# Optimization experiments

Measured on AMD Instinct MI355X. Metric: run time of the kernel, lower is better.

## Reference

```python
import jax, jax.numpy as jnp
import numpy as np

MAX_VAL = 1000000000000.0


def setup_inputs() -> dict:
    key = jax.random.key(0)
    k1, k2, k3, k4 = jax.random.split(key, 4)
    B, H, N, D = 2, 16, 2048, 64
    query = jax.random.normal(k1, (B, H, N, D), dtype=jnp.float32)
    key_t = jax.random.normal(k2, (B, H, N, D), dtype=jnp.float32)
    value = jax.random.normal(k3, (B, H, N, D), dtype=jnp.float32)
    mask = jax.random.randint(k4, (B, 1, 1, N), 0, 2).astype(bool)
    return {"query": query, "key": key_t, "value": value, "mask": mask,
            "global_num": 8, "window_size": 64}


def reference(query, key, value, mask, global_num, window_size):
    # query/key/value: [B, H, N, D]; mask: [B, 1, 1, N] bool (True = keep)
    B, H, N, D = query.shape
    scale = 1.0 / jnp.sqrt(jnp.asarray(D, dtype=query.dtype))

    # split heads: first global_num are global, rest are local (windowed)
    q_g, k_g, v_g = query[:, :global_num], key[:, :global_num], value[:, :global_num]
    q_l, k_l, v_l = query[:, global_num:], key[:, global_num:], value[:, global_num:]

    # ---- global heads: dense masked attention ----
    scores_g = jnp.einsum('bhqd,bhkd->bhqk', q_g, k_g) * scale
    scores_g = jnp.where(mask, scores_g, -MAX_VAL)
    p_g = jax.nn.softmax(scores_g, axis=-1)
    out_g = jnp.einsum('bhqk,bhkd->bhqd', p_g, v_l[:, :0]) if False else jnp.einsum('bhqk,bhkd->bhqd', p_g, v_g)

    # ---- local heads: window-banded mask on top of padding mask ----
    pos = jnp.arange(N)
    distance = jnp.abs(pos[None, :] - pos[:, None])  # [N, N]
    band = (distance <= window_size)                 # [N, N] bool
    mask_l = mask & band                             # [B, 1, N, N]
    scores_l = jnp.einsum('bhqd,bhkd->bhqk', q_l, k_l) * scale
    scores_l = jnp.where(mask_l, scores_l, -MAX_VAL)
    p_l = jax.nn.softmax(scores_l, axis=-1)
    out_l = jnp.einsum('bhqk,bhkd->bhqd', p_l, v_l)

    out = jnp.concatenate([out_g, out_l], axis=1)  # [B, H, N, D]
    return (out, p_g, p_l)
```

## Files before the change

### kernel.cpp

```cpp
#include <hip/hip_runtime.h>
#include <stdint.h>

typedef __attribute__((ext_vector_type(8))) __bf16 bf16x8;
typedef __attribute__((ext_vector_type(4))) float f32x4;
typedef __attribute__((ext_vector_type(4))) int i32x4;

#define DEVI static __device__ __forceinline__

constexpr int NN = 2048;
constexpr int DD = 64;
constexpr int NH = 16;
constexpr int NG = 8;
constexpr float SCALE = 0.125f;
constexpr float NEGBIG = -1.0e12f;
constexpr size_t OUT_ELEMS = (size_t)2 * NH * NN * DD;
constexpr size_t PG_ELEMS  = (size_t)2 * NG * NN * NN;
constexpr size_t T_ELEMS   = (size_t)2 * NH * NN * DD;
constexpr size_t WS_NEED   = 5 * T_ELEMS * sizeof(__bf16);

struct Frag { bf16x8 hi, lo; };

DEVI Frag make_frag(const float* p) {
  f32x4 a = *(const f32x4*)p;
  f32x4 b = *(const f32x4*)(p + 4);
  Frag f;
#pragma unroll
  for (int j = 0; j < 8; j++) {
    float x = (j < 4) ? a[j] : b[j - 4];
    __bf16 h = (__bf16)x;
    f.hi[j] = h;
    f.lo[j] = (__bf16)(x - (float)h);
  }
  return f;
}

DEVI f32x4 mfma(bf16x8 a, bf16x8 b, f32x4 c) {
  return __builtin_amdgcn_mfma_f32_16x16x32_bf16(a, b, c, 0, 0, 0);
}

DEVI void nt_store4(float* p, f32x4 v) {
  __builtin_nontemporal_store(v, (f32x4*)p);
}

struct KT { bf16x8 hi[2][2]; bf16x8 lo[2][2]; i32x4 mv[2]; };
struct VT { bf16x8 v[4]; };

template <bool PRE>
DEVI void load_kt(KT& kt, const __bf16* khi, const __bf16* klo,
                  const float* kp, const int* mp, int wc, int li, int qi) {
#pragma unroll
  for (int Mt = 0; Mt < 2; Mt++)
#pragma unroll
    for (int ks = 0; ks < 2; ks++) {
      const size_t off = (size_t)(wc + Mt * 16 + li) * DD + ks * 32 + qi * 8;
      if constexpr (PRE) {
        kt.hi[Mt][ks] = *(const bf16x8*)(khi + off);
        kt.lo[Mt][ks] = *(const bf16x8*)(klo + off);
      } else {
        Frag f = make_frag(kp + off);
        kt.hi[Mt][ks] = f.hi;
        kt.lo[Mt][ks] = f.lo;
      }
    }
  kt.mv[0] = *(const i32x4*)(mp + wc + qi * 4);
  kt.mv[1] = *(const i32x4*)(mp + wc + 16 + qi * 4);
}

template <bool PRE>
DEVI void load_vt(VT& vt, const __bf16* vtp, const float* vp, int wc, int li, int qi) {
  if constexpr (PRE) {
#pragma unroll
    for (int dt = 0; dt < 4; dt++)
      vt.v[dt] = *(const bf16x8*)(vtp + (size_t)(dt * 16 + li) * NN + wc + qi * 8);
  } else {
#pragma unroll
    for (int dt = 0; dt < 4; dt++)
#pragma unroll
      for (int j = 0; j < 8; j++)
        vt.v[dt][j] = (__bf16)vp[(size_t)(wc + qi * 8 + j) * DD + dt * 16 + li];
  }
}

template <bool LOC>
DEVI void tileA(const KT& kt, const Frag qf[2][2], int wc, int rb, int li, int qi,
                float* m, float* l) {
#pragma unroll
  for (int rs = 0; rs < 2; rs++) {
    f32x4 acc[2];
#pragma unroll
    for (int Mt = 0; Mt < 2; Mt++) {
      f32x4 c = {0.f, 0.f, 0.f, 0.f};
#pragma unroll
      for (int ks = 0; ks < 2; ks++) {
        c = mfma(kt.hi[Mt][ks], qf[rs][ks].hi, c);
        c = mfma(kt.hi[Mt][ks], qf[rs][ks].lo, c);
        c = mfma(kt.lo[Mt][ks], qf[rs][ks].hi, c);
      }
      acc[Mt] = c;
    }
    const int row = rb + rs * 16 + li;
    float vals[8];
#pragma unroll
    for (int Mt = 0; Mt < 2; Mt++)
#pragma unroll
      for (int r = 0; r < 4; r++) {
        const int col = wc + Mt * 16 + qi * 4 + r;
        bool ok = (kt.mv[Mt][r] != 0);
        if constexpr (LOC) { int d = row - col; if (d < 0) d = -d; ok = ok && (d <= 64); }
        vals[Mt * 4 + r] = ok ? acc[Mt][r] * SCALE : NEGBIG;
      }
    float mx = vals[0];
#pragma unroll
    for (int j = 1; j < 8; j++) mx = fmaxf(mx, vals[j]);
    const float mn = fmaxf(m[rs], mx);
    float s = 0.f;
#pragma unroll
    for (int j = 0; j < 8; j++) s += __expf(vals[j] - mn);
    l[rs] = l[rs] * __expf(m[rs] - mn) + s;
    m[rs] = mn;
  }
}

template <bool LOC>
DEVI void tileB(const KT& kt, const VT& vt, const Frag qf[2][2], int wc, int rb,
                int li, int qi, const float* m, const float* rl,
                f32x4 (&o)[2][4], float* pp, int srcA, int srcB, bool selB) {
#pragma unroll
  for (int rs = 0; rs < 2; rs++) {
    f32x4 acc[2];
#pragma unroll
    for (int Mt = 0; Mt < 2; Mt++) {
      f32x4 c = {0.f, 0.f, 0.f, 0.f};
#pragma unroll
      for (int ks = 0; ks < 2; ks++) {
        c = mfma(kt.hi[Mt][ks], qf[rs][ks].hi, c);
        c = mfma(kt.hi[Mt][ks], qf[rs][ks].lo, c);
        c = mfma(kt.lo[Mt][ks], qf[rs][ks].hi, c);
      }
      acc[Mt] = c;
    }
    const int row = rb + rs * 16 + li;
    float pf[8];
#pragma unroll
    for (int Mt = 0; Mt < 2; Mt++)
#pragma unroll
      for (int r = 0; r < 4; r++) {
        const int col = wc + Mt * 16 + qi * 4 + r;
        bool ok = (kt.mv[Mt][r] != 0);
        if constexpr (LOC) { int d = row - col; if (d < 0) d = -d; ok = ok && (d <= 64); }
        const float vv = ok ? acc[Mt][r] * SCALE : NEGBIG;
        pf[Mt * 4 + r] = __expf(vv - m[rs]) * rl[rs];
      }
    float pa[8];
#pragma unroll
    for (int j = 0; j < 8; j++) {
      const int src = (j < 4) ? srcA : srcB;
      const float v0 = __shfl(pf[0 + (j & 3)], src);
      const float v1 = __shfl(pf[4 + (j & 3)], src);
      pa[j] = selB ? v1 : v0;
    }
    float* prow = pp + (size_t)(rb + rs * 16 + li) * NN + wc + qi * 8;
    nt_store4(prow,     (f32x4){pa[0], pa[1], pa[2], pa[3]});
    nt_store4(prow + 4, (f32x4){pa[4], pa[5], pa[6], pa[7]});
    bf16x8 pb;
#pragma unroll
    for (int j = 0; j < 8; j++) pb[j] = (__bf16)pa[j];
#pragma unroll
    for (int dt = 0; dt < 4; dt++)
      o[rs][dt] = mfma(pb, vt.v[dt], o[rs][dt]);
  }
}

__global__ __launch_bounds__(256)
void prep(const float* __restrict__ Q, const float* __restrict__ K,
          const float* __restrict__ V, __bf16* __restrict__ W) {
  const int bid = blockIdx.x;
  if (bid < 4096) {
    const float* src = (bid < 2048) ? Q : K;
    __bf16* hi = W + ((bid < 2048) ? (size_t)0 : 2 * T_ELEMS);
    __bf16* lo = hi + T_ELEMS;
    const size_t base = ((size_t)(bid & 2047) * 256 + threadIdx.x) * 8;
    f32x4 a = *(const f32x4*)(src + base);
    f32x4 b = *(const f32x4*)(src + base + 4);
    bf16x8 h, l;
#pragma unroll
    for (int j = 0; j < 8; j++) {
      float x = (j < 4) ? a[j] : b[j - 4];
      __bf16 hh = (__bf16)x;
      h[j] = hh;
      l[j] = (__bf16)(x - (float)hh);
    }
    *(bf16x8*)(hi + base) = h;
    *(bf16x8*)(lo + base) = l;
  } else {
    __bf16* vt = W + 4 * T_ELEMS;
    const int t  = (bid - 4096) * 256 + (int)threadIdx.x;
    const int ng = t & 63;
    const int dh = t >> 6;
    const int d  = dh & 63;
    const int bh = dh >> 6;
    const float* vp = V + (size_t)bh * NN * DD;
    __bf16* dst = vt + ((size_t)bh * DD + d) * NN + ng * 32;
    bf16x8 o[4];
#pragma unroll
    for (int j = 0; j < 32; j++)
      o[j >> 3][j & 7] = (__bf16)vp[(size_t)(ng * 32 + j) * DD + d];
#pragma unroll
    for (int k = 0; k < 4; k++) *(bf16x8*)(dst + k * 8) = o[k];
  }
}

template <bool PRE>
__global__ __launch_bounds__(256, 4)
void wattn(const float* __restrict__ Q, const float* __restrict__ K,
           const float* __restrict__ V, const int* __restrict__ MSK,
           float* __restrict__ OUT, const __bf16* __restrict__ W) {
  __shared__ float2 mlS[4][32];
  __shared__ float  oS[4][16][64];

  const int bid0 = (int)blockIdx.x;
  const int xcd = bid0 & 7, jj = bid0 >> 3;
  const int bid = (jj < 128) ? (xcd * 128 + jj) : (1024 + xcd * 128 + (jj - 128));
  const bool loc = bid >= 1024;
  const int lb = loc ? bid - 1024 : bid;
  const int bh = lb >> 6;
  const int b  = bh >> 3;
  const int hh = bh & 7;
  const int h  = loc ? (hh + 8) : hh;
  const int rb = (lb & 63) * 32;
  const int wave = (int)(threadIdx.x >> 6);
  const int lane = (int)(threadIdx.x & 63);
  const int qi = lane >> 4;
  const int li = lane & 15;

  const size_t tb = ((size_t)(b * NH + h) * NN) * DD;
  const float* qp = Q + tb;
  const float* kp = K + tb;
  const float* vp = V + tb;
  const __bf16* qhi = W + tb;
  const __bf16* qlo = W + T_ELEMS + tb;
  const __bf16* khi = W + 2 * T_ELEMS + tb;
  const __bf16* klo = W + 3 * T_ELEMS + tb;
  const __bf16* vtp = W + 4 * T_ELEMS + (size_t)(b * NH + h) * DD * NN;
  const int*   mp = MSK + (size_t)b * NN;
  float* op = OUT + tb;
  float* pp = OUT + OUT_ELEMS + (loc ? PG_ELEMS : (size_t)0)
                  + ((size_t)(b * NG + hh) * NN) * NN;

  const int cb  = rb - 64;
  const int wlo = cb < 0 ? 0 : cb;
  const int whi = (rb + 96 > NN) ? NN : rb + 96;

  if (loc) {
    const int c0 = (int)threadIdx.x * 8;
    const f32x4 z = {0.f, 0.f, 0.f, 0.f};
#pragma unroll 1
    for (int rr = 0; rr < 32; rr++) {
      if (c0 >= wlo && c0 < whi) continue;
      float* dst = pp + (size_t)(rb + rr) * NN + c0;
      nt_store4(dst, z);
      nt_store4(dst + 4, z);
    }
  }

  Frag qf[2][2];
#pragma unroll
  for (int rs = 0; rs < 2; rs++)
#pragma unroll
    for (int ks = 0; ks < 2; ks++) {
      const size_t off = (size_t)(rb + rs * 16 + li) * DD + ks * 32 + qi * 8;
      if constexpr (PRE) {
        qf[rs][ks].hi = *(const bf16x8*)(qhi + off);
        qf[rs][ks].lo = *(const bf16x8*)(qlo + off);
      } else {
        qf[rs][ks] = make_frag(qp + off);
      }
    }

  float m[2] = {NEGBIG, NEGBIG};
  float l[2] = {0.f, 0.f};

  if (!loc) {
#pragma unroll 1
    for (int tt = 0; tt < 16; tt++) {
      const int wc = wave * 512 + tt * 32;
      KT kt;
      load_kt<PRE>(kt, khi, klo, kp, mp, wc, li, qi);
      tileA<false>(kt, qf, wc, rb, li, qi, m, l);
    }
  } else {
#pragma unroll 1
    for (int t = wave; t < 5; t += 4) {
      const int wc = cb + 32 * t;
      if ((unsigned)wc >= (unsigned)NN) continue;
      KT kt;
      load_kt<PRE>(kt, khi, klo, kp, mp, wc, li, qi);
      tileA<true>(kt, qf, wc, rb, li, qi, m, l);
    }
  }

#pragma unroll
  for (int rs = 0; rs < 2; rs++) {
#pragma unroll
    for (int off = 16; off <= 32; off <<= 1) {
      const float mo  = __shfl_xor(m[rs], off);
      const float lo2 = __shfl_xor(l[rs], off);
      const float mn  = fmaxf(m[rs], mo);
      l[rs] = l[rs] * __expf(m[rs] - mn) + lo2 * __expf(mo - mn);
      m[rs] = mn;
    }
    if (qi == 0) mlS[wave][rs * 16 + li] = make_float2(m[rs], l[rs]);
  }
  __syncthreads();

  float rl[2];
#pragma unroll
  for (int rs = 0; rs < 2; rs++) {
    float mm = NEGBIG, ll = 0.f;
#pragma unroll
    for (int w = 0; w < 4; w++) {
      const float2 p = mlS[w][rs * 16 + li];
      const float mn = fmaxf(mm, p.x);
      ll = ll * __expf(mm - mn) + p.y * __expf(p.x - mn);
      mm = mn;
    }
    m[rs] = mm;
    rl[rs] = 1.0f / ll;
  }

  f32x4 o[2][4];
#pragma unroll
  for (int rs = 0; rs < 2; rs++)
#pragma unroll
    for (int dt = 0; dt < 4; dt++) o[rs][dt] = (f32x4){0.f, 0.f, 0.f, 0.f};

  const int srcA = (((qi * 2) + 0) & 3) * 16 + li;
  const int srcB = (((qi * 2) + 1) & 3) * 16 + li;
  const bool selB = (qi >> 1) != 0;

  if (!loc) {
#pragma unroll 1
    for (int tt = 0; tt < 16; tt++) {
      const int wc = wave * 512 + tt * 32;
      KT kt;
      VT vt;
      load_kt<PRE>(kt, khi, klo, kp, mp, wc, li, qi);
      load_vt<PRE>(vt, vtp, vp, wc, li, qi);
      tileB<false>(kt, vt, qf, wc, rb, li, qi, m, rl, o, pp, srcA, srcB, selB);
    }
  } else {
#pragma unroll 1
    for (int t = wave; t < 5; t += 4) {
      const int wc = cb + 32 * t;
      if ((unsigned)wc >= (unsigned)NN) continue;
      KT kt;
      VT vt;
      load_kt<PRE>(kt, khi, klo, kp, mp, wc, li, qi);
      load_vt<PRE>(vt, vtp, vp, wc, li, qi);
      tileB<true>(kt, vt, qf, wc, rb, li, qi, m, rl, o, pp, srcA, srcB, selB);
    }
  }

  const int tid = (int)threadIdx.x;
  const int rr = tid >> 4;
  const int d0 = (tid & 15) * 4;
#pragma unroll
  for (int rs = 0; rs < 2; rs++) {
#pragma unroll
    for (int dt = 0; dt < 4; dt++)
#pragma unroll
      for (int r = 0; r < 4; r++)
        oS[wave][qi * 4 + r][dt * 16 + li] = o[rs][dt][r];
    __syncthreads();
    f32x4 s = {0.f, 0.f, 0.f, 0.f};
#pragma unroll
    for (int w = 0; w < 4; w++)
      s += *(const f32x4*)&oS[w][rr][d0];
    nt_store4(op + (size_t)(rb + rs * 16 + rr) * DD + d0, s);
    if (rs == 0) __syncthreads();
  }
}

extern "C" void kernel_launch(void* const* d_in, const int* in_sizes, int n_in,
                              void* d_out, int out_size, void* d_ws, size_t ws_size,
                              hipStream_t stream) {
  (void)in_sizes; (void)n_in; (void)out_size;
  const float* Q = (const float*)d_in[0];
  const float* K = (const float*)d_in[1];
  const float* V = (const float*)d_in[2];
  const int*   M = (const int*)d_in[3];
  float* O = (float*)d_out;
  if (ws_size >= WS_NEED && d_ws != nullptr) {
    __bf16* W = (__bf16*)d_ws;
    prep<<<dim3(4608), dim3(256), 0, stream>>>(Q, K, V, W);
    wattn<true><<<dim3(2048), dim3(256), 0, stream>>>(Q, K, V, M, O, W);
  } else {
    wattn<false><<<dim3(2048), dim3(256), 0, stream>>>(Q, K, V, M, O, nullptr);
  }
}
```

Before: 861.4 us.

## Split pass-B into per-row-subtile loops and use regular stores for outputs

The second pass now loops over the two 16-row subtiles one at a time, reloading only that subtile's Q fragments and keeping four output accumulators instead of eight. This lowers register pressure so occupancy can rise, but K/V tiles and the mask are loaded twice. Nontemporal stores for the probability matrices and the output are also replaced with ordinary stores.

New measurement: 888.9 us. 1.03x slower.

```diff
diff --git a/kernel.cpp b/kernel.cpp
--- a/kernel.cpp
+++ b/kernel.cpp
@@ -38,10 +38,6 @@
   return __builtin_amdgcn_mfma_f32_16x16x32_bf16(a, b, c, 0, 0, 0);
 }
 
-DEVI void nt_store4(float* p, f32x4 v) {
-  __builtin_nontemporal_store(v, (f32x4*)p);
-}
-
 struct KT { bf16x8 hi[2][2]; bf16x8 lo[2][2]; i32x4 mv[2]; };
 struct VT { bf16x8 v[4]; };
 
@@ -82,7 +78,7 @@
 }
 
 template <bool LOC>
-DEVI void tileA(const KT& kt, const Frag qf[2][2], int wc, int rb, int li, int qi,
+DEVI void tileA(const KT& kt, const Frag qa[2][2], int wc, int rb, int li, int qi,
                 float* m, float* l) {
 #pragma unroll
   for (int rs = 0; rs < 2; rs++) {
@@ -92,9 +88,9 @@
       f32x4 c = {0.f, 0.f, 0.f, 0.f};
 #pragma unroll
       for (int ks = 0; ks < 2; ks++) {
-        c = mfma(kt.hi[Mt][ks], qf[rs][ks].hi, c);
-        c = mfma(kt.hi[Mt][ks], qf[rs][ks].lo, c);
-        c = mfma(kt.lo[Mt][ks], qf[rs][ks].hi, c);
+        c = mfma(kt.hi[Mt][ks], qa[rs][ks].hi, c);
+        c = mfma(kt.hi[Mt][ks], qa[rs][ks].lo, c);
+        c = mfma(kt.lo[Mt][ks], qa[rs][ks].hi, c);
       }
       acc[Mt] = c;
     }
@@ -122,53 +118,50 @@
 }
 
 template <bool LOC>
-DEVI void tileB(const KT& kt, const VT& vt, const Frag qf[2][2], int wc, int rb,
-                int li, int qi, const float* m, const float* rl,
-                f32x4 (&o)[2][4], float* pp, int srcA, int srcB, bool selB) {
-#pragma unroll
-  for (int rs = 0; rs < 2; rs++) {
-    f32x4 acc[2];
-#pragma unroll
-    for (int Mt = 0; Mt < 2; Mt++) {
-      f32x4 c = {0.f, 0.f, 0.f, 0.f};
-#pragma unroll
-      for (int ks = 0; ks < 2; ks++) {
-        c = mfma(kt.hi[Mt][ks], qf[rs][ks].hi, c);
-        c = mfma(kt.hi[Mt][ks], qf[rs][ks].lo, c);
-        c = mfma(kt.lo[Mt][ks], qf[rs][ks].hi, c);
-      }
-      acc[Mt] = c;
-    }
-    const int row = rb + rs * 16 + li;
-    float pf[8];
-#pragma unroll
-    for (int Mt = 0; Mt < 2; Mt++)
-#pragma unroll
-      for (int r = 0; r < 4; r++) {
-        const int col = wc + Mt * 16 + qi * 4 + r;
-        bool ok = (kt.mv[Mt][r] != 0);
-        if constexpr (LOC) { int d = row - col; if (d < 0) d = -d; ok = ok && (d <= 64); }
-        const float vv = ok ? acc[Mt][r] * SCALE : NEGBIG;
-        pf[Mt * 4 + r] = __expf(vv - m[rs]) * rl[rs];
-      }
-    float pa[8];
-#pragma unroll
-    for (int j = 0; j < 8; j++) {
-      const int src = (j < 4) ? srcA : srcB;
-      const float v0 = __shfl(pf[0 + (j & 3)], src);
-      const float v1 = __shfl(pf[4 + (j & 3)], src);
-      pa[j] = selB ? v1 : v0;
-    }
-    float* prow = pp + (size_t)(rb + rs * 16 + li) * NN + wc + qi * 8;
-    nt_store4(prow,     (f32x4){pa[0], pa[1], pa[2], pa[3]});
-    nt_store4(prow + 4, (f32x4){pa[4], pa[5], pa[6], pa[7]});
-    bf16x8 pb;
-#pragma unroll
-    for (int j = 0; j < 8; j++) pb[j] = (__bf16)pa[j];
-#pragma unroll
-    for (int dt = 0; dt < 4; dt++)
-      o[rs][dt] = mfma(pb, vt.v[dt], o[rs][dt]);
-  }
+DEVI void tileB1(const KT& kt, const VT& vt, const Frag qb[2], int wc, int row0,
+                 int li, int qi, float mm, float rl1, f32x4 (&o)[4],
+                 float* pp, int srcA, int srcB, bool selB) {
+  f32x4 acc[2];
+#pragma unroll
+  for (int Mt = 0; Mt < 2; Mt++) {
+    f32x4 c = {0.f, 0.f, 0.f, 0.f};
+#pragma unroll
+    for (int ks = 0; ks < 2; ks++) {
+      c = mfma(kt.hi[Mt][ks], qb[ks].hi, c);
+      c = mfma(kt.hi[Mt][ks], qb[ks].lo, c);
+      c = mfma(kt.lo[Mt][ks], qb[ks].hi, c);
+    }
+    acc[Mt] = c;
+  }
+  const int row = row0 + li;
+  float pf[8];
+#pragma unroll
+  for (int Mt = 0; Mt < 2; Mt++)
+#pragma unroll
+    for (int r = 0; r < 4; r++) {
+      const int col = wc + Mt * 16 + qi * 4 + r;
+      bool ok = (kt.mv[Mt][r] != 0);
+      if constexpr (LOC) { int d = row - col; if (d < 0) d = -d; ok = ok && (d <= 64); }
+      const float vv = ok ? acc[Mt][r] * SCALE : NEGBIG;
+      pf[Mt * 4 + r] = __expf(vv - mm) * rl1;
+    }
+  float pa[8];
+#pragma unroll
+  for (int j = 0; j < 8; j++) {
+    const int src = (j < 4) ? srcA : srcB;
+    const float v0 = __shfl(pf[0 + (j & 3)], src);
+    const float v1 = __shfl(pf[4 + (j & 3)], src);
+    pa[j] = selB ? v1 : v0;
+  }
+  float* prow = pp + (size_t)row * NN + wc + qi * 8;
+  *(f32x4*)prow       = (f32x4){pa[0], pa[1], pa[2], pa[3]};
+  *(f32x4*)(prow + 4) = (f32x4){pa[4], pa[5], pa[6], pa[7]};
+  bf16x8 pb;
+#pragma unroll
+  for (int j = 0; j < 8; j++) pb[j] = (__bf16)pa[j];
+#pragma unroll
+  for (int dt = 0; dt < 4; dt++)
+    o[dt] = mfma(pb, vt.v[dt], o[dt]);
 }
 
 __global__ __launch_bounds__(256)
@@ -258,44 +251,46 @@
     for (int rr = 0; rr < 32; rr++) {
       if (c0 >= wlo && c0 < whi) continue;
       float* dst = pp + (size_t)(rb + rr) * NN + c0;
-      nt_store4(dst, z);
-      nt_store4(dst + 4, z);
-    }
-  }
-
-  Frag qf[2][2];
-#pragma unroll
-  for (int rs = 0; rs < 2; rs++)
-#pragma unroll
-    for (int ks = 0; ks < 2; ks++) {
-      const size_t off = (size_t)(rb + rs * 16 + li) * DD + ks * 32 + qi * 8;
-      if constexpr (PRE) {
-        qf[rs][ks].hi = *(const bf16x8*)(qhi + off);
-        qf[rs][ks].lo = *(const bf16x8*)(qlo + off);
-      } else {
-        qf[rs][ks] = make_frag(qp + off);
-      }
-    }
+      *(f32x4*)dst       = z;
+      *(f32x4*)(dst + 4) = z;
+    }
+  }
 
   float m[2] = {NEGBIG, NEGBIG};
   float l[2] = {0.f, 0.f};
 
-  if (!loc) {
-#pragma unroll 1
-    for (int tt = 0; tt < 16; tt++) {
-      const int wc = wave * 512 + tt * 32;
-      KT kt;
-      load_kt<PRE>(kt, khi, klo, kp, mp, wc, li, qi);
-      tileA<false>(kt, qf, wc, rb, li, qi, m, l);
-    }
-  } else {
-#pragma unroll 1
-    for (int t = wave; t < 5; t += 4) {
-      const int wc = cb + 32 * t;
-      if ((unsigned)wc >= (unsigned)NN) continue;
-      KT kt;
-      load_kt<PRE>(kt, khi, klo, kp, mp, wc, li, qi);
-      tileA<true>(kt, qf, wc, rb, li, qi, m, l);
+  {
+    Frag qa[2][2];
+#pragma unroll
+    for (int rs = 0; rs < 2; rs++)
+#pragma unroll
+      for (int ks = 0; ks < 2; ks++) {
+        const size_t off = (size_t)(rb + rs * 16 + li) * DD + ks * 32 + qi * 8;
+        if constexpr (PRE) {
+          qa[rs][ks].hi = *(const bf16x8*)(qhi + off);
+          qa[rs][ks].lo = *(const bf16x8*)(qlo + off);
+        } else {
+          qa[rs][ks] = make_frag(qp + off);
+        }
+      }
+
+    if (!loc) {
+#pragma unroll 1
+      for (int tt = 0; tt < 16; tt++) {
+        const int wc = wave * 512 + tt * 32;
+        KT kt;
+        load_kt<PRE>(kt, khi, klo, kp, mp, wc, li, qi);
+        tileA<false>(kt, qa, wc, rb, li, qi, m, l);
+      }
+    } else {
+#pragma unroll 1
+      for (int t = wave; t < 5; t += 4) {
+        const int wc = cb + 32 * t;
+        if ((unsigned)wc >= (unsigned)NN) continue;
+        KT kt;
+        load_kt<PRE>(kt, khi, klo, kp, mp, wc, li, qi);
+        tileA<true>(kt, qa, wc, rb, li, qi, m, l);
+      }
     }
   }
 
@@ -328,55 +323,68 @@
     rl[rs] = 1.0f / ll;
   }
 
-  f32x4 o[2][4];
-#pragma unroll
-  for (int rs = 0; rs < 2; rs++)
-#pragma unroll
-    for (int dt = 0; dt < 4; dt++) o[rs][dt] = (f32x4){0.f, 0.f, 0.f, 0.f};
-
   const int srcA = (((qi * 2) + 0) & 3) * 16 + li;
   const int srcB = (((qi * 2) + 1) & 3) * 16 + li;
   const bool selB = (qi >> 1) != 0;
-
-  if (!loc) {
-#pragma unroll 1
-    for (int tt = 0; tt < 16; tt++) {
-      const int wc = wave * 512 + tt * 32;
-      KT kt;
-      VT vt;
-      load_kt<PRE>(kt, khi, klo, kp, mp, wc, li, qi);
-      load_vt<PRE>(vt, vtp, vp, wc, li, qi);
-      tileB<false>(kt, vt, qf, wc, rb, li, qi, m, rl, o, pp, srcA, srcB, selB);
-    }
-  } else {
-#pragma unroll 1
-    for (int t = wave; t < 5; t += 4) {
-      const int wc = cb + 32 * t;
-      if ((unsigned)wc >= (unsigned)NN) continue;
-      KT kt;
-      VT vt;
-      load_kt<PRE>(kt, khi, klo, kp, mp, wc, li, qi);
-      load_vt<PRE>(vt, vtp, vp, wc, li, qi);
-      tileB<true>(kt, vt, qf, wc, rb, li, qi, m, rl, o, pp, srcA, srcB, selB);
-    }
-  }
-
   const int tid = (int)threadIdx.x;
   const int rr = tid >> 4;
   const int d0 = (tid & 15) * 4;
-#pragma unroll
+
+#pragma unroll 1
   for (int rs = 0; rs < 2; rs++) {
+    const int row0 = rb + rs * 16;
+    Frag qb[2];
+#pragma unroll
+    for (int ks = 0; ks < 2; ks++) {
+      const size_t off = (size_t)(row0 + li) * DD + ks * 32 + qi * 8;
+      if constexpr (PRE) {
+        qb[ks].hi = *(const bf16x8*)(qhi + off);
+        qb[ks].lo = *(const bf16x8*)(qlo + off);
+      } else {
+        qb[ks] = make_frag(qp + off);
+      }
+    }
+
+    f32x4 o[4];
+#pragma unroll
+    for (int dt = 0; dt < 4; dt++) o[dt] = (f32x4){0.f, 0.f, 0.f, 0.f};
+
+    if (!loc) {
+#pragma unroll 1
+      for (int tt = 0; tt < 16; tt++) {
+        const int wc = wave * 512 + tt * 32;
+        KT kt;
+        VT vt;
+        load_kt<PRE>(kt, khi, klo, kp, mp, wc, li, qi);
+        load_vt<PRE>(vt, vtp, vp, wc, li, qi);
+        tileB1<false>(kt, vt, qb, wc, row0, li, qi, m[rs], rl[rs], o, pp,
+                      srcA, srcB, selB);
+      }
+    } else {
+#pragma unroll 1
+      for (int t = wave; t < 5; t += 4) {
+        const int wc = cb + 32 * t;
+        if ((unsigned)wc >= (unsigned)NN) continue;
+        KT kt;
+        VT vt;
+        load_kt<PRE>(kt, khi, klo, kp, mp, wc, li, qi);
+        load_vt<PRE>(vt, vtp, vp, wc, li, qi);
+        tileB1<true>(kt, vt, qb, wc, row0, li, qi, m[rs], rl[rs], o, pp,
+                     srcA, srcB, selB);
+      }
+    }
+
 #pragma unroll
     for (int dt = 0; dt < 4; dt++)
 #pragma unroll
       for (int r = 0; r < 4; r++)
-        oS[wave][qi * 4 + r][dt * 16 + li] = o[rs][dt][r];
+        oS[wave][qi * 4 + r][dt * 16 + li] = o[dt][r];
     __syncthreads();
     f32x4 s = {0.f, 0.f, 0.f, 0.f};
 #pragma unroll
     for (int w = 0; w < 4; w++)
       s += *(const f32x4*)&oS[w][rr][d0];
-    nt_store4(op + (size_t)(rb + rs * 16 + rr) * DD + d0, s);
+    *(f32x4*)(op + (size_t)(row0 + rr) * DD + d0) = s;
     if (rs == 0) __syncthreads();
   }
 }
```
